# Kernel optimization log

Measured on AMD Instinct MI355X. Metric: run time of the kernel, lower is better.

## Reference

```python
import jax, jax.numpy as jnp
import numpy as np

N, E = 50000, 800000
IN_DIM, HID, HEADS, EDGE_DIM, OUT_DIM = 329, 64, 4, 2, 1
NEG_SLOPE = 0.2


def setup_inputs() -> dict:
    key = jax.random.key(0)
    ks = jax.random.split(key, 20)
    p = lambda k, shp: (jax.random.normal(k, shp, dtype=jnp.float32) * 0.1)
    inp = {
        'x': jax.random.normal(ks[0], (N, IN_DIM), dtype=jnp.float32),
        'edge_attr': jax.random.normal(ks[1], (E, EDGE_DIM), dtype=jnp.float32),
        'edge_index': jax.random.randint(ks[2], (2, E), 0, N, dtype=jnp.int32),
        # conv1: GATConv(329 -> 64, heads=4, edge_dim=2), concat=True
        'W1': p(ks[3], (IN_DIM, HEADS * HID)),
        'att_src1': p(ks[4], (HEADS, HID)),
        'att_dst1': p(ks[5], (HEADS, HID)),
        'We1': p(ks[6], (EDGE_DIM, HEADS * HID)),
        'att_e1': p(ks[7], (HEADS, HID)),
        'b1': jnp.zeros((HEADS * HID,), jnp.float32),
        # conv2: GATConv(256 -> 64, heads=1, edge_dim=2), concat=True
        'W2': p(ks[8], (HEADS * HID, HID)),
        'att_src2': p(ks[9], (1, HID)),
        'att_dst2': p(ks[10], (1, HID)),
        'We2': p(ks[11], (EDGE_DIM, HID)),
        'att_e2': p(ks[12], (1, HID)),
        'b2': jnp.zeros((HID,), jnp.float32),
        # fc head
        'Wf': p(ks[13], (HID, OUT_DIM)),
        'bf': jnp.zeros((OUT_DIM,), jnp.float32),
    }
    return inp


def gat_conv(x, src, dst, ea, W, att_src, att_dst, We, att_e, bias, heads, out_ch):
    n = x.shape[0]
    h = (x @ W).reshape(n, heads, out_ch)                    # [N,H,C]
    a_src = (h * att_src).sum(-1)                            # [N,H]
    a_dst = (h * att_dst).sum(-1)                            # [N,H]
    e = (ea @ We).reshape(-1, heads, out_ch)                 # [Et,H,C]
    a_e = (e * att_e).sum(-1)                                # [Et,H]
    alpha = a_src[src] + a_dst[dst] + a_e                    # [Et,H]
    alpha = jnp.where(alpha > 0, alpha, NEG_SLOPE * alpha)   # leaky_relu
    amax = jax.ops.segment_max(alpha, dst, num_segments=n)
    ex = jnp.exp(alpha - amax[dst])
    denom = jax.ops.segment_sum(ex, dst, num_segments=n)
    attn = ex / (denom[dst] + 1e-16)                         # [Et,H]
    out = jax.ops.segment_sum(attn[..., None] * h[src], dst, num_segments=n)
    return out.reshape(n, heads * out_ch) + bias


def reference(x, edge_attr, edge_index, W1, att_src1, att_dst1, We1, att_e1, b1,
              W2, att_src2, att_dst2, We2, att_e2, b2, Wf, bf):
    n = x.shape[0]
    # add_self_loops with fill_value='mean' for edge_attr (PyG GATConv default)
    loop = jnp.arange(n, dtype=edge_index.dtype)
    src = jnp.concatenate([edge_index[0], loop])
    dst = jnp.concatenate([edge_index[1], loop])
    mean_ea = jnp.mean(edge_attr, axis=0)
    ea = jnp.concatenate([edge_attr, jnp.broadcast_to(mean_ea, (n, edge_attr.shape[1]))])
    h = gat_conv(x, src, dst, ea, W1, att_src1, att_dst1, We1, att_e1, b1, HEADS, HID)
    h = jax.nn.elu(h)
    h = gat_conv(h, src, dst, ea, W2, att_src2, att_dst2, We2, att_e2, b2, 1, HID)
    out = h @ Wf + bf
    return out.squeeze(-1)
```

## Files before the change

### kernel.cpp

```cpp
#include <hip/hip_runtime.h>
#include <hip/hip_bf16.h>
#include <math.h>


#define DEVFN __device__ __forceinline__

typedef __attribute__((ext_vector_type(8))) short short8;
typedef __attribute__((ext_vector_type(4))) float f32x4;

DEVFN float wave_reduce_sum(float v) {
    for (int off = 32; off; off >>= 1) v += __shfl_xor(v, off);
    return v;
}

DEVFN ushort f2bf_rne(float f) {
    unsigned u = __float_as_uint(f);
    unsigned r = (u + 0x7fff + ((u >> 16) & 1)) >> 16;
    return (ushort)r;
}
DEVFN float bf2f(ushort b) { return __uint_as_float(((unsigned)b) << 16); }

__global__ void k_init(int* __restrict__ deg, float* __restrict__ meanbuf, int N) {
    int i = blockIdx.x * blockDim.x + threadIdx.x;
    if (i < N) deg[i] = 0;
    if (i < 2) meanbuf[i] = 0.f;
}

__global__ void k_count(const int* __restrict__ dstrow, int* __restrict__ deg,
                        int* __restrict__ rank, int E, int Et) {
    int t = blockIdx.x * blockDim.x + threadIdx.x;
    if (t >= Et) return;
    int d = (t < E) ? dstrow[t] : (t - E);
    rank[t] = atomicAdd(&deg[d], 1);
}

__global__ void k_mean(const float* __restrict__ ea, float* __restrict__ meanbuf, int E) {
    __shared__ float s0s[4], s1s[4];
    float s0 = 0.f, s1 = 0.f;
    for (int i = blockIdx.x * blockDim.x + threadIdx.x; i < E; i += gridDim.x * blockDim.x) {
        float2 v = reinterpret_cast<const float2*>(ea)[i];
        s0 += v.x; s1 += v.y;
    }
    s0 = wave_reduce_sum(s0);
    s1 = wave_reduce_sum(s1);
    int lane = threadIdx.x & 63, w = threadIdx.x >> 6;
    if (lane == 0) { s0s[w] = s0; s1s[w] = s1; }
    __syncthreads();
    if (threadIdx.x == 0) {
        float a = 0.f, b = 0.f;
        for (int i = 0; i < (int)(blockDim.x >> 6); i++) { a += s0s[i]; b += s1s[i]; }
        atomicAdd(&meanbuf[0], a);
        atomicAdd(&meanbuf[1], b);
    }
}

__global__ void k_scan_block(const int* __restrict__ deg, int* __restrict__ rowptr,
                             int* __restrict__ bsums, int N) {
    __shared__ int sd[1024];
    int i = blockIdx.x * 1024 + threadIdx.x;
    sd[threadIdx.x] = (i < N) ? deg[i] : 0;
    __syncthreads();
    for (int off = 1; off < 1024; off <<= 1) {
        int x = (threadIdx.x >= off) ? sd[threadIdx.x - off] : 0;
        __syncthreads();
        sd[threadIdx.x] += x;
        __syncthreads();
    }
    if (i < N) rowptr[i + 1] = sd[threadIdx.x];
    if (threadIdx.x == 1023) bsums[blockIdx.x] = sd[1023];
}

__global__ void k_scan_bsums(const int* __restrict__ bsums, int* __restrict__ boffs, int nb) {
    if (threadIdx.x == 0 && blockIdx.x == 0) {
        int run = 0;
        for (int b = 0; b < nb; b++) { boffs[b] = run; run += bsums[b]; }
    }
}

__global__ void k_scan_finalize(int* __restrict__ rowptr, const int* __restrict__ boffs, int N) {
    int i = blockIdx.x * blockDim.x + threadIdx.x;
    if (i < N) rowptr[i + 1] += boffs[i >> 10];
    if (i == 0) rowptr[0] = 0;
}

__global__ void k_fill(const int* __restrict__ srcrow, const int* __restrict__ dstrow,
                       const int* __restrict__ rowptr, const int* __restrict__ rank,
                       int* __restrict__ srcid, float2* __restrict__ ea_csr,
                       const float* __restrict__ ea, const float* __restrict__ meanbuf,
                       float invE, int E, int Et) {
    int t = blockIdx.x * blockDim.x + threadIdx.x;
    if (t >= Et) return;
    int d, s; float2 ev;
    if (t < E) {
        d = dstrow[t]; s = srcrow[t];
        ev = reinterpret_cast<const float2*>(ea)[t];
    } else {
        d = t - E; s = t - E;
        ev = make_float2(meanbuf[0] * invE, meanbuf[1] * invE);
    }
    int pos = rowptr[d] + rank[t];
    srcid[pos] = s;
    ea_csr[pos] = ev;
}

template <int H>
__global__ void k_collapse(const float* __restrict__ We, const float* __restrict__ att_e,
                           float* __restrict__ M) {
    int t = threadIdx.x;
    int lane = t & 63, w = t >> 6;
    int d = w / H, h = w % H;
    float v = We[(d * H + h) * 64 + lane] * att_e[h * 64 + lane];
    v = wave_reduce_sum(v);
    if (lane == 0) M[d * H + h] = v;
}

__global__ void k_split_wT(const float* __restrict__ W, ushort* __restrict__ hiT,
                           ushort* __restrict__ loT, int K, int Nc, int Kpad) {
    int c = blockIdx.x;
    for (int k = threadIdx.x; k < Kpad; k += blockDim.x) {
        float v = (k < K) ? W[(size_t)k * Nc + c] : 0.f;
        ushort h = f2bf_rne(v);
        ushort l = f2bf_rne(v - bf2f(h));
        hiT[(size_t)c * Kpad + k] = h;
        loT[(size_t)c * Kpad + k] = l;
    }
}

template <int MI, int NI>
__global__ __launch_bounds__(256) void k_gemm_mfma(const float* __restrict__ A,
                                                   const ushort* __restrict__ BhT,
                                                   const ushort* __restrict__ BlT,
                                                   float* __restrict__ C,
                                                   ushort* __restrict__ Cbf,
                                                   int M, int K, int Kpad, int ldc) {
    constexpr int BM = 32 * MI, BN = 32 * NI;
    constexpr int LDA = 40;
    __shared__ __align__(16) ushort Ah[BM * LDA];
    __shared__ __align__(16) ushort Al[BM * LDA];
    __shared__ __align__(16) ushort Bh[BN * LDA];
    __shared__ __align__(16) ushort Bl[BN * LDA];

    int tid = threadIdx.x, lane = tid & 63, wid = tid >> 6;
    int wr = wid >> 1, wc = wid & 1;
    int bm = blockIdx.x * BM, bn = blockIdx.y * BN;

    f32x4 acc[MI][NI];
#pragma unroll
    for (int mi = 0; mi < MI; ++mi)
#pragma unroll
        for (int ni = 0; ni < NI; ++ni) acc[mi][ni] = (f32x4){0.f, 0.f, 0.f, 0.f};

    int steps = Kpad / 32;
    for (int s = 0; s < steps; ++s) {
        int k0 = s * 32;
        __syncthreads();
#pragma unroll
        for (int j = 0; j < BM / 32; ++j) {
            int slot = tid + 256 * j;
            int row = slot >> 3, ch = slot & 7;
            int gr = bm + row, kb = k0 + ch * 4;
            float v[4];
#pragma unroll
            for (int e = 0; e < 4; ++e) {
                int kk = kb + e;
                v[e] = (gr < M && kk < K) ? A[(size_t)gr * K + kk] : 0.f;
            }
            ushort h[4], l[4];
#pragma unroll
            for (int e = 0; e < 4; ++e) {
                h[e] = f2bf_rne(v[e]);
                l[e] = f2bf_rne(v[e] - bf2f(h[e]));
            }
            *reinterpret_cast<ushort4*>(&Ah[row * LDA + ch * 4]) = make_ushort4(h[0], h[1], h[2], h[3]);
            *reinterpret_cast<ushort4*>(&Al[row * LDA + ch * 4]) = make_ushort4(l[0], l[1], l[2], l[3]);
        }
#pragma unroll
        for (int j = 0; j < BN / 64; ++j) {
            int slot = tid + 256 * j;
            int n = slot >> 2, ch = slot & 3;
            size_t goff = (size_t)(bn + n) * Kpad + k0 + ch * 8;
            *reinterpret_cast<float4*>(&Bh[n * LDA + ch * 8]) =
                *reinterpret_cast<const float4*>(&BhT[goff]);
            *reinterpret_cast<float4*>(&Bl[n * LDA + ch * 8]) =
                *reinterpret_cast<const float4*>(&BlT[goff]);
        }
        __syncthreads();
        int kg = (lane >> 4) * 8;
        int am = wr * (MI * 16) + (lane & 15);
        int bc = wc * (NI * 16) + (lane & 15);
        short8 ah[MI], al[MI], bh[NI], bl[NI];
#pragma unroll
        for (int mi = 0; mi < MI; ++mi) {
            ah[mi] = *reinterpret_cast<const short8*>(&Ah[(am + mi * 16) * LDA + kg]);
            al[mi] = *reinterpret_cast<const short8*>(&Al[(am + mi * 16) * LDA + kg]);
        }
#pragma unroll
        for (int ni = 0; ni < NI; ++ni) {
            bh[ni] = *reinterpret_cast<const short8*>(&Bh[(bc + ni * 16) * LDA + kg]);
            bl[ni] = *reinterpret_cast<const short8*>(&Bl[(bc + ni * 16) * LDA + kg]);
        }
#pragma unroll
        for (int mi = 0; mi < MI; ++mi)
#pragma unroll
            for (int ni = 0; ni < NI; ++ni) {
                acc[mi][ni] = __builtin_amdgcn_mfma_f32_16x16x32_bf16(ah[mi], bh[ni], acc[mi][ni], 0, 0, 0);
                acc[mi][ni] = __builtin_amdgcn_mfma_f32_16x16x32_bf16(ah[mi], bl[ni], acc[mi][ni], 0, 0, 0);
                acc[mi][ni] = __builtin_amdgcn_mfma_f32_16x16x32_bf16(al[mi], bh[ni], acc[mi][ni], 0, 0, 0);
            }
    }
#pragma unroll
    for (int mi = 0; mi < MI; ++mi) {
        int row0 = bm + wr * (MI * 16) + mi * 16 + ((lane >> 4) << 2);
#pragma unroll
        for (int ni = 0; ni < NI; ++ni) {
            int col = bn + wc * (NI * 16) + ni * 16 + (lane & 15);
            f32x4 v = acc[mi][ni];
#pragma unroll
            for (int r = 0; r < 4; ++r)
                if (row0 + r < M) {
                    C[(size_t)(row0 + r) * ldc + col] = v[r];
                    Cbf[(size_t)(row0 + r) * ldc + col] = f2bf_rne(v[r]);
                }
        }
    }
}

template <int H>
__global__ void k_node_attn(const float* __restrict__ h, const float* __restrict__ att_src,
                            const float* __restrict__ att_dst, float* __restrict__ asrc,
                            float* __restrict__ adst, int N) {
    constexpr int HC = H * 64;
    constexpr int NPB = 256 / HC;
    int local = threadIdx.x % HC;
    int n = blockIdx.x * NPB + threadIdx.x / HC;
    if (n >= N) return;
    float v = h[(size_t)n * HC + local];
    float s = v * att_src[local];
    float d = v * att_dst[local];
    for (int off = 32; off; off >>= 1) { s += __shfl_xor(s, off); d += __shfl_xor(d, off); }
    if ((local & 63) == 0) {
        int hh = local >> 6;
        asrc[n * H + hh] = s;
        adst[n * H + hh] = d;
    }
}

template <int H>
__global__ void k_attn(const int* __restrict__ rowptr, const int* __restrict__ srcid,
                       const float2* __restrict__ ea_csr, const float* __restrict__ asrc,
                       const float* __restrict__ adst, const float* __restrict__ M,
                       float* __restrict__ attn, float* __restrict__ dinv, int N) {
    int lane = threadIdx.x & 63;
    int n = blockIdx.x * 4 + (threadIdx.x >> 6);
    if (n >= N) return;
    int start = rowptr[n];
    int items = (rowptr[n + 1] - start) * H;
    int h = lane % H;
    float ad = adst[n * H + h];
    float m0 = M[h], m1 = M[H + h];

    float mx = -1e30f;
    for (int i = lane; i < items; i += 64) {
        int p = start + i / H;
        int s = srcid[p];
        float2 ev = ea_csr[p];
        float al = asrc[s * H + h] + ad + ev.x * m0 + ev.y * m1;
        al = (al > 0.f) ? al : 0.2f * al;
        attn[(size_t)start * H + i] = al;
        mx = fmaxf(mx, al);
    }
    for (int off = H; off < 64; off <<= 1) mx = fmaxf(mx, __shfl_xor(mx, off));

    float ss = 0.f;
    for (int i = lane; i < items; i += 64) {
        float ex = expf(attn[(size_t)start * H + i] - mx);
        attn[(size_t)start * H + i] = ex;
        ss += ex;
    }
    for (int off = H; off < 64; off <<= 1) ss += __shfl_xor(ss, off);
    if (lane < H) dinv[n * H + h] = 1.f / (ss + 1e-16f);
}

template <int H, bool ELU>
__global__ void k_aggregate_bf(const int* __restrict__ rowptr, const int* __restrict__ srcid,
                               const float* __restrict__ attn, const float* __restrict__ dinv,
                               const ushort* __restrict__ hbf, const float* __restrict__ bias,
                               float* __restrict__ out, int N) {
    constexpr int HC = H * 64;
    constexpr int LPN = HC / 8;
    constexpr int NPB = 256 / LPN;
    int li = threadIdx.x % LPN;
    int n = blockIdx.x * NPB + threadIdx.x / LPN;
    if (n >= N) return;
    int hh = li >> 3;
    const short8* h8 = reinterpret_cast<const short8*>(hbf);
    int start = rowptr[n], end = rowptr[n + 1];
    float acc[8];
#pragma unroll
    for (int j = 0; j < 8; ++j) acc[j] = 0.f;
    int p = start;
    for (; p + 3 < end; p += 4) {
        int s0 = srcid[p], s1 = srcid[p + 1], s2 = srcid[p + 2], s3 = srcid[p + 3];
        float w0 = attn[p * H + hh], w1 = attn[(p + 1) * H + hh];
        float w2 = attn[(p + 2) * H + hh], w3 = attn[(p + 3) * H + hh];
        short8 v0 = h8[(size_t)s0 * LPN + li];
        short8 v1 = h8[(size_t)s1 * LPN + li];
        short8 v2 = h8[(size_t)s2 * LPN + li];
        short8 v3 = h8[(size_t)s3 * LPN + li];
#pragma unroll
        for (int j = 0; j < 8; ++j)
            acc[j] += w0 * bf2f((ushort)v0[j]) + w1 * bf2f((ushort)v1[j]) +
                      w2 * bf2f((ushort)v2[j]) + w3 * bf2f((ushort)v3[j]);
    }
    for (; p < end; ++p) {
        int s = srcid[p];
        float w = attn[p * H + hh];
        short8 v = h8[(size_t)s * LPN + li];
#pragma unroll
        for (int j = 0; j < 8; ++j) acc[j] += w * bf2f((ushort)v[j]);
    }
    float inv = dinv[n * H + hh];
    const float4* b4 = reinterpret_cast<const float4*>(bias);
    float4 ba = b4[li * 2], bb = b4[li * 2 + 1];
    float bv[8] = {ba.x, ba.y, ba.z, ba.w, bb.x, bb.y, bb.z, bb.w};
    float4 o0, o1;
#pragma unroll
    for (int j = 0; j < 8; ++j) {
        float r = acc[j] * inv + bv[j];
        if (ELU) r = (r > 0.f) ? r : expm1f(r);
        ((j < 4) ? (&o0.x) : (&o1.x))[j & 3] = r;
    }
    float4* out4 = reinterpret_cast<float4*>(out);
    out4[(size_t)n * (HC / 4) + li * 2]     = o0;
    out4[(size_t)n * (HC / 4) + li * 2 + 1] = o1;
}

__global__ void k_aggregate_fc(const int* __restrict__ rowptr, const int* __restrict__ srcid,
                               const float* __restrict__ attn, const float* __restrict__ dinv,
                               const ushort* __restrict__ hbf, const float* __restrict__ bias,
                               const float* __restrict__ Wf, const float* __restrict__ bf,
                               float* __restrict__ out, int N) {
    constexpr int LPN = 8;
    int li = threadIdx.x % LPN;
    int n = blockIdx.x * 32 + threadIdx.x / LPN;
    if (n >= N) return;
    const short8* h8 = reinterpret_cast<const short8*>(hbf);
    int start = rowptr[n], end = rowptr[n + 1];
    float acc[8];
#pragma unroll
    for (int j = 0; j < 8; ++j) acc[j] = 0.f;
    int p = start;
    for (; p + 3 < end; p += 4) {
        int s0 = srcid[p], s1 = srcid[p + 1], s2 = srcid[p + 2], s3 = srcid[p + 3];
        float w0 = attn[p], w1 = attn[p + 1], w2 = attn[p + 2], w3 = attn[p + 3];
        short8 v0 = h8[(size_t)s0 * LPN + li];
        short8 v1 = h8[(size_t)s1 * LPN + li];
        short8 v2 = h8[(size_t)s2 * LPN + li];
        short8 v3 = h8[(size_t)s3 * LPN + li];
#pragma unroll
        for (int j = 0; j < 8; ++j)
            acc[j] += w0 * bf2f((ushort)v0[j]) + w1 * bf2f((ushort)v1[j]) +
                      w2 * bf2f((ushort)v2[j]) + w3 * bf2f((ushort)v3[j]);
    }
    for (; p < end; ++p) {
        int s = srcid[p];
        float w = attn[p];
        short8 v = h8[(size_t)s * LPN + li];
#pragma unroll
        for (int j = 0; j < 8; ++j) acc[j] += w * bf2f((ushort)v[j]);
    }
    float inv = dinv[n];
    const float4* b4 = reinterpret_cast<const float4*>(bias);
    const float4* w4 = reinterpret_cast<const float4*>(Wf);
    float4 ba = b4[li * 2], bb = b4[li * 2 + 1];
    float4 wa = w4[li * 2], wb = w4[li * 2 + 1];
    float bv[8] = {ba.x, ba.y, ba.z, ba.w, bb.x, bb.y, bb.z, bb.w};
    float wv[8] = {wa.x, wa.y, wa.z, wa.w, wb.x, wb.y, wb.z, wb.w};
    float partial = 0.f;
#pragma unroll
    for (int j = 0; j < 8; ++j) partial += (acc[j] * inv + bv[j]) * wv[j];
    partial += __shfl_xor(partial, 1);
    partial += __shfl_xor(partial, 2);
    partial += __shfl_xor(partial, 4);
    if (li == 0) out[n] = partial + bf[0];
}

extern "C" void kernel_launch(void* const* d_in, const int* in_sizes, int n_in,
                              void* d_out, int out_size, void* d_ws, size_t ws_size,
                              hipStream_t stream) {
    const float* x        = (const float*)d_in[0];
    const float* ea       = (const float*)d_in[1];
    const int*   ei       = (const int*)d_in[2];
    const float* W1       = (const float*)d_in[3];
    const float* att_src1 = (const float*)d_in[4];
    const float* att_dst1 = (const float*)d_in[5];
    const float* We1      = (const float*)d_in[6];
    const float* att_e1   = (const float*)d_in[7];
    const float* b1       = (const float*)d_in[8];
    const float* W2       = (const float*)d_in[9];
    const float* att_src2 = (const float*)d_in[10];
    const float* att_dst2 = (const float*)d_in[11];
    const float* We2      = (const float*)d_in[12];
    const float* att_e2   = (const float*)d_in[13];
    const float* b2       = (const float*)d_in[14];
    const float* Wf       = (const float*)d_in[15];
    const float* bf       = (const float*)d_in[16];

    const int IN_DIM = 329;
    const int K1PAD = 352;
    int N  = in_sizes[0] / IN_DIM;
    int E  = in_sizes[1] / 2;
    int Et = E + N;
    const int* srcrow = ei;
    const int* dstrow = ei + E;

    char* p = (char*)d_ws;
    size_t used = 0;
    auto alloc = [&](size_t bytes) -> void* {
        void* r = p;
        size_t pad = (bytes + 255) & ~(size_t)255;
        p += pad; used += pad;
        return r;
    };
    float*  h1     = (float*)alloc((size_t)N * 256 * 4);
    float*  agg1   = (float*)alloc((size_t)N * 256 * 4);
    ushort* h1bf   = (ushort*)alloc((size_t)N * 256 * 2);
    ushort* h2bf   = (ushort*)alloc((size_t)N * 64 * 2);
    float*  asrc   = (float*)alloc((size_t)N * 4 * 4);
    float*  adst   = (float*)alloc((size_t)N * 4 * 4);
    float*  dinv   = (float*)alloc((size_t)N * 4 * 4);
    float*  attn   = (float*)alloc((size_t)Et * 4 * 4);
    float2* ea_csr = (float2*)alloc((size_t)Et * 8);
    int*    srcid  = (int*)alloc((size_t)Et * 4);
    int*    rank   = (int*)alloc((size_t)Et * 4);
    ushort* w1hT   = (ushort*)alloc((size_t)256 * K1PAD * 2);
    ushort* w1lT   = (ushort*)alloc((size_t)256 * K1PAD * 2);
    ushort* w2hT   = (ushort*)alloc((size_t)64 * 256 * 2);
    ushort* w2lT   = (ushort*)alloc((size_t)64 * 256 * 2);
    float*  M1     = (float*)alloc(256);
    float*  M2     = (float*)alloc(256);
    float*  meanbuf= (float*)alloc(256);
    int*    rowptr = (int*)alloc((size_t)(N + 1) * 4);
    int*    deg    = (int*)alloc((size_t)N * 4);
    int*    bsums  = (int*)alloc(1024);
    int*    boffs  = (int*)alloc(1024);
    if (used > ws_size) return;

    int gN  = (N + 255) / 256;
    int gEt = (Et + 255) / 256;
    int nb  = (N + 1023) / 1024;
    int gM  = (N + 127) / 128;
    float invE = 1.f / (float)E;

    k_init<<<gN, 256, 0, stream>>>(deg, meanbuf, N);
    k_count<<<gEt, 256, 0, stream>>>(dstrow, deg, rank, E, Et);
    k_mean<<<256, 256, 0, stream>>>(ea, meanbuf, E);
    k_scan_block<<<nb, 1024, 0, stream>>>(deg, rowptr, bsums, N);
    k_scan_bsums<<<1, 64, 0, stream>>>(bsums, boffs, nb);
    k_scan_finalize<<<gN, 256, 0, stream>>>(rowptr, boffs, N);
    k_fill<<<gEt, 256, 0, stream>>>(srcrow, dstrow, rowptr, rank, srcid, ea_csr, ea,
                                    meanbuf, invE, E, Et);

    k_collapse<4><<<1, 512, 0, stream>>>(We1, att_e1, M1);
    k_collapse<1><<<1, 128, 0, stream>>>(We2, att_e2, M2);
    k_split_wT<<<256, 384, 0, stream>>>(W1, w1hT, w1lT, IN_DIM, 256, K1PAD);
    k_split_wT<<<64, 256, 0, stream>>>(W2, w2hT, w2lT, 256, 64, 256);

    k_gemm_mfma<4, 4><<<dim3(gM, 2), 256, 0, stream>>>(x, w1hT, w1lT, h1, h1bf, N, IN_DIM, K1PAD, 256);
    k_node_attn<4><<<N, 256, 0, stream>>>(h1, att_src1, att_dst1, asrc, adst, N);
    k_attn<4><<<(N + 3) / 4, 256, 0, stream>>>(rowptr, srcid, ea_csr, asrc, adst, M1, attn, dinv, N);
    k_aggregate_bf<4, true><<<(N + 7) / 8, 256, 0, stream>>>(rowptr, srcid, attn, dinv,
                                                             h1bf, b1, agg1, N);

    k_gemm_mfma<4, 2><<<dim3(gM, 1), 256, 0, stream>>>(agg1, w2hT, w2lT, h1 , h2bf, N, 256, 256, 64);
    k_node_attn<1><<<(N + 3) / 4, 256, 0, stream>>>(h1, att_src2, att_dst2, asrc, adst, N);
    k_attn<1><<<(N + 3) / 4, 256, 0, stream>>>(rowptr, srcid, ea_csr, asrc, adst, M2, attn, dinv, N);
    k_aggregate_fc<<<(N + 31) / 32, 256, 0, stream>>>(rowptr, srcid, attn, dinv,
                                                      h2bf, b2, Wf, bf, (float*)d_out, N);
}
```

Before: 483.2 us.

## Pre-split GEMM inputs into bf16 hi/lo planes and store activations as planes

Adds a kernel that splits x into padded bf16 hi/lo planes once, so the GEMM loads pre-converted tiles with vector loads instead of converting fp32 in its inner loop. The GEMM outputs and the layer-1 aggregation now write bf16 hi/lo planes instead of fp32 plus bf16 copies. Workspace buffers are reused across layers, and the GEMM tile shapes and grids change. The goal is less fp32 traffic and less conversion work, at the cost of an extra split pass over x and rows read past N in the padded buffer (those rows are never initialized).

```diff
diff --git a/kernel.cpp b/kernel.cpp
--- a/kernel.cpp
+++ b/kernel.cpp
@@ -126,13 +126,25 @@
     }
 }
 
+__global__ void k_split_a(const float* __restrict__ A, ushort* __restrict__ Ah,
+                          ushort* __restrict__ Al, int K, int Kpad) {
+    int row = blockIdx.x;
+    for (int k = threadIdx.x; k < Kpad; k += blockDim.x) {
+        float v = (k < K) ? A[(size_t)row * K + k] : 0.f;
+        ushort h = f2bf_rne(v);
+        Ah[(size_t)row * Kpad + k] = h;
+        Al[(size_t)row * Kpad + k] = f2bf_rne(v - bf2f(h));
+    }
+}
+
 template <int MI, int NI>
-__global__ __launch_bounds__(256) void k_gemm_mfma(const float* __restrict__ A,
-                                                   const ushort* __restrict__ BhT,
-                                                   const ushort* __restrict__ BlT,
-                                                   float* __restrict__ C,
-                                                   ushort* __restrict__ Cbf,
-                                                   int M, int K, int Kpad, int ldc) {
+__global__ __launch_bounds__(256) void k_gemm_pre(const ushort* __restrict__ Agh,
+                                                  const ushort* __restrict__ Agl,
+                                                  const ushort* __restrict__ BhT,
+                                                  const ushort* __restrict__ BlT,
+                                                  ushort* __restrict__ Ch,
+                                                  ushort* __restrict__ Cl,
+                                                  int M, int Kpad, int ldc) {
     constexpr int BM = 32 * MI, BN = 32 * NI;
     constexpr int LDA = 40;
     __shared__ __align__(16) ushort Ah[BM * LDA];
@@ -155,34 +167,24 @@
         int k0 = s * 32;
         __syncthreads();
 #pragma unroll
-        for (int j = 0; j < BM / 32; ++j) {
+        for (int j = 0; j < (BM * 4) / 256; ++j) {
             int slot = tid + 256 * j;
-            int row = slot >> 3, ch = slot & 7;
-            int gr = bm + row, kb = k0 + ch * 4;
-            float v[4];
-#pragma unroll
-            for (int e = 0; e < 4; ++e) {
-                int kk = kb + e;
-                v[e] = (gr < M && kk < K) ? A[(size_t)gr * K + kk] : 0.f;
-            }
-            ushort h[4], l[4];
-#pragma unroll
-            for (int e = 0; e < 4; ++e) {
-                h[e] = f2bf_rne(v[e]);
-                l[e] = f2bf_rne(v[e] - bf2f(h[e]));
-            }
-            *reinterpret_cast<ushort4*>(&Ah[row * LDA + ch * 4]) = make_ushort4(h[0], h[1], h[2], h[3]);
-            *reinterpret_cast<ushort4*>(&Al[row * LDA + ch * 4]) = make_ushort4(l[0], l[1], l[2], l[3]);
+            int row = slot >> 2, ch = slot & 3;
+            size_t g = (size_t)(bm + row) * Kpad + k0 + ch * 8;
+            *reinterpret_cast<float4*>(&Ah[row * LDA + ch * 8]) =
+                *reinterpret_cast<const float4*>(&Agh[g]);
+            *reinterpret_cast<float4*>(&Al[row * LDA + ch * 8]) =
+                *reinterpret_cast<const float4*>(&Agl[g]);
         }
 #pragma unroll
-        for (int j = 0; j < BN / 64; ++j) {
+        for (int j = 0; j < (BN * 4) / 256; ++j) {
             int slot = tid + 256 * j;
             int n = slot >> 2, ch = slot & 3;
-            size_t goff = (size_t)(bn + n) * Kpad + k0 + ch * 8;
+            size_t g = (size_t)(bn + n) * Kpad + k0 + ch * 8;
             *reinterpret_cast<float4*>(&Bh[n * LDA + ch * 8]) =
-                *reinterpret_cast<const float4*>(&BhT[goff]);
+                *reinterpret_cast<const float4*>(&BhT[g]);
             *reinterpret_cast<float4*>(&Bl[n * LDA + ch * 8]) =
-                *reinterpret_cast<const float4*>(&BlT[goff]);
+                *reinterpret_cast<const float4*>(&BlT[g]);
         }
         __syncthreads();
         int kg = (lane >> 4) * 8;
@@ -218,30 +220,33 @@
 #pragma unroll
             for (int r = 0; r < 4; ++r)
                 if (row0 + r < M) {
-                    C[(size_t)(row0 + r) * ldc + col] = v[r];
-                    Cbf[(size_t)(row0 + r) * ldc + col] = f2bf_rne(v[r]);
+                    ushort hb = f2bf_rne(v[r]);
+                    Ch[(size_t)(row0 + r) * ldc + col] = hb;
+                    Cl[(size_t)(row0 + r) * ldc + col] = f2bf_rne(v[r] - bf2f(hb));
                 }
         }
     }
 }
 
 template <int H>
-__global__ void k_node_attn(const float* __restrict__ h, const float* __restrict__ att_src,
-                            const float* __restrict__ att_dst, float* __restrict__ asrc,
-                            float* __restrict__ adst, int N) {
+__global__ void k_node_attn2(const ushort* __restrict__ hh, const ushort* __restrict__ hl,
+                             const float* __restrict__ att_src,
+                             const float* __restrict__ att_dst, float* __restrict__ asrc,
+                             float* __restrict__ adst, int N) {
     constexpr int HC = H * 64;
     constexpr int NPB = 256 / HC;
     int local = threadIdx.x % HC;
     int n = blockIdx.x * NPB + threadIdx.x / HC;
     if (n >= N) return;
-    float v = h[(size_t)n * HC + local];
+    size_t idx = (size_t)n * HC + local;
+    float v = bf2f(hh[idx]) + bf2f(hl[idx]);
     float s = v * att_src[local];
     float d = v * att_dst[local];
     for (int off = 32; off; off >>= 1) { s += __shfl_xor(s, off); d += __shfl_xor(d, off); }
     if ((local & 63) == 0) {
-        int hh = local >> 6;
-        asrc[n * H + hh] = s;
-        adst[n * H + hh] = d;
+        int hhid = local >> 6;
+        asrc[n * H + hhid] = s;
+        adst[n * H + hhid] = d;
     }
 }
 
@@ -281,11 +286,11 @@
     if (lane < H) dinv[n * H + h] = 1.f / (ss + 1e-16f);
 }
 
-template <int H, bool ELU>
-__global__ void k_aggregate_bf(const int* __restrict__ rowptr, const int* __restrict__ srcid,
-                               const float* __restrict__ attn, const float* __restrict__ dinv,
-                               const ushort* __restrict__ hbf, const float* __restrict__ bias,
-                               float* __restrict__ out, int N) {
+template <int H>
+__global__ void k_aggregate_planes(const int* __restrict__ rowptr, const int* __restrict__ srcid,
+                                   const float* __restrict__ attn, const float* __restrict__ dinv,
+                                   const ushort* __restrict__ hbf, const float* __restrict__ bias,
+                                   ushort* __restrict__ outh, ushort* __restrict__ outl, int N) {
     constexpr int HC = H * 64;
     constexpr int LPN = HC / 8;
     constexpr int NPB = 256 / LPN;
@@ -323,16 +328,17 @@
     const float4* b4 = reinterpret_cast<const float4*>(bias);
     float4 ba = b4[li * 2], bb = b4[li * 2 + 1];
     float bv[8] = {ba.x, ba.y, ba.z, ba.w, bb.x, bb.y, bb.z, bb.w};
-    float4 o0, o1;
+    short8 oh, ol;
 #pragma unroll
     for (int j = 0; j < 8; ++j) {
         float r = acc[j] * inv + bv[j];
-        if (ELU) r = (r > 0.f) ? r : expm1f(r);
-        ((j < 4) ? (&o0.x) : (&o1.x))[j & 3] = r;
-    }
-    float4* out4 = reinterpret_cast<float4*>(out);
-    out4[(size_t)n * (HC / 4) + li * 2]     = o0;
-    out4[(size_t)n * (HC / 4) + li * 2 + 1] = o1;
+        r = (r > 0.f) ? r : expm1f(r);
+        ushort hb = f2bf_rne(r);
+        oh[j] = (short)hb;
+        ol[j] = (short)f2bf_rne(r - bf2f(hb));
+    }
+    reinterpret_cast<short8*>(outh)[(size_t)n * LPN + li] = oh;
+    reinterpret_cast<short8*>(outl)[(size_t)n * LPN + li] = ol;
 }
 
 __global__ void k_aggregate_fc(const int* __restrict__ rowptr, const int* __restrict__ srcid,
@@ -414,6 +420,10 @@
     const int* srcrow = ei;
     const int* dstrow = ei + E;
 
+    int gM1  = (N + 127) / 128;
+    int gM2  = (N + 63) / 64;
+    int Mpad = gM1 * 128;
+
     char* p = (char*)d_ws;
     size_t used = 0;
     auto alloc = [&](size_t bytes) -> void* {
@@ -422,10 +432,16 @@
         p += pad; used += pad;
         return r;
     };
-    float*  h1     = (float*)alloc((size_t)N * 256 * 4);
-    float*  agg1   = (float*)alloc((size_t)N * 256 * 4);
-    ushort* h1bf   = (ushort*)alloc((size_t)N * 256 * 2);
-    ushort* h2bf   = (ushort*)alloc((size_t)N * 64 * 2);
+    ushort* bufA   = (ushort*)alloc((size_t)Mpad * K1PAD * 2 * 2);
+    ushort* xh     = bufA;
+    ushort* xl     = bufA + (size_t)Mpad * K1PAD;
+    ushort* aggh   = bufA;
+    ushort* aggl   = bufA + (size_t)Mpad * 256;
+    ushort* bufB   = (ushort*)alloc((size_t)N * 256 * 2 * 2);
+    ushort* h1h    = bufB;
+    ushort* h1l    = bufB + (size_t)N * 256;
+    ushort* h2h    = bufB;
+    ushort* h2l    = bufB + (size_t)N * 64;
     float*  asrc   = (float*)alloc((size_t)N * 4 * 4);
     float*  adst   = (float*)alloc((size_t)N * 4 * 4);
     float*  dinv   = (float*)alloc((size_t)N * 4 * 4);
@@ -449,7 +465,6 @@
     int gN  = (N + 255) / 256;
     int gEt = (Et + 255) / 256;
     int nb  = (N + 1023) / 1024;
-    int gM  = (N + 127) / 128;
     float invE = 1.f / (float)E;
 
     k_init<<<gN, 256, 0, stream>>>(deg, meanbuf, N);
@@ -465,16 +480,19 @@
     k_collapse<1><<<1, 128, 0, stream>>>(We2, att_e2, M2);
     k_split_wT<<<256, 384, 0, stream>>>(W1, w1hT, w1lT, IN_DIM, 256, K1PAD);
     k_split_wT<<<64, 256, 0, stream>>>(W2, w2hT, w2lT, 256, 64, 256);
-
-    k_gemm_mfma<4, 4><<<dim3(gM, 2), 256, 0, stream>>>(x, w1hT, w1lT, h1, h1bf, N, IN_DIM, K1PAD, 256);
-    k_node_attn<4><<<N, 256, 0, stream>>>(h1, att_src1, att_dst1, asrc, adst, N);
+    k_split_a<<<N, 384, 0, stream>>>(x, xh, xl, IN_DIM, K1PAD);
+
+    k_gemm_pre<4, 2><<<dim3(gM1, 4), 256, 0, stream>>>(xh, xl, w1hT, w1lT, h1h, h1l,
+                                                       N, K1PAD, 256);
+    k_node_attn2<4><<<N, 256, 0, stream>>>(h1h, h1l, att_src1, att_dst1, asrc, adst, N);
     k_attn<4><<<(N + 3) / 4, 256, 0, stream>>>(rowptr, srcid, ea_csr, asrc, adst, M1, attn, dinv, N);
-    k_aggregate_bf<4, true><<<(N + 7) / 8, 256, 0, stream>>>(rowptr, srcid, attn, dinv,
-                                                             h1bf, b1, agg1, N);
-
-    k_gemm_mfma<4, 2><<<dim3(gM, 1), 256, 0, stream>>>(agg1, w2hT, w2lT, h1 , h2bf, N, 256, 256, 64);
-    k_node_attn<1><<<(N + 3) / 4, 256, 0, stream>>>(h1, att_src2, att_dst2, asrc, adst, N);
+    k_aggregate_planes<4><<<(N + 7) / 8, 256, 0, stream>>>(rowptr, srcid, attn, dinv,
+                                                           h1h, b1, aggh, aggl, N);
+
+    k_gemm_pre<2, 2><<<dim3(gM2, 1), 256, 0, stream>>>(aggh, aggl, w2hT, w2lT, h2h, h2l,
+                                                       N, 256, 64);
+    k_node_attn2<1><<<(N + 3) / 4, 256, 0, stream>>>(h2h, h2l, att_src2, att_dst2, asrc, adst, N);
     k_attn<1><<<(N + 3) / 4, 256, 0, stream>>>(rowptr, srcid, ea_csr, asrc, adst, M2, attn, dinv, N);
     k_aggregate_fc<<<(N + 31) / 32, 256, 0, stream>>>(rowptr, srcid, attn, dinv,
-                                                      h2bf, b2, Wf, bf, (float*)d_out, N);
-}
+                                                      h2h, b2, Wf, bf, (float*)d_out, N);
+}
```

New measurement: 510.4 us. 1.06x slower.
